# Kernel tuning notes

Measured on AMD Instinct MI355X. Metric: run time of the kernel, lower is better.

The kernel has to match this reference:

```python
import jax, jax.numpy as jnp
import numpy as np

B, C, L = 8, 2048, 256          # batch, seq (EEG channels), feature length
E = 3 * L                        # embed_dim = 768 (fused QKV width)
H = 4                            # attention heads
D = E // (3 * H)                 # head_dim = 64
SCALE = 8.0                      # hardcoded in the module (== sqrt(D) here)


def _layer_norm(x, gamma, beta, eps=1e-5):
    mu = jnp.mean(x, axis=-1, keepdims=True)
    var = jnp.var(x, axis=-1, keepdims=True)
    return (x - mu) * jax.lax.rsqrt(var + eps) * gamma + beta


def setup_inputs() -> dict:
    key = jax.random.key(0)
    ks = jax.random.split(key, 5)
    x = jax.random.normal(ks[0], (B, C, L), dtype=jnp.float32)
    # layers_1: Linear(L -> E) + LayerNorm(E)
    W1 = jax.random.normal(ks[1], (L, E), dtype=jnp.float32) / np.sqrt(L)
    b1 = jnp.zeros((E,), dtype=jnp.float32)
    g1 = jnp.ones((E,), dtype=jnp.float32)
    beta1 = jnp.zeros((E,), dtype=jnp.float32)
    # layers_2: Linear(L -> L) + LayerNorm(L)
    W2 = jax.random.normal(ks[2], (L, L), dtype=jnp.float32) / np.sqrt(L)
    b2 = jnp.zeros((L,), dtype=jnp.float32)
    g2 = jnp.ones((L,), dtype=jnp.float32)
    beta2 = jnp.zeros((L,), dtype=jnp.float32)
    return {"x": x, "W1": W1, "b1": b1, "g1": g1, "beta1": beta1,
            "W2": W2, "b2": b2, "g2": g2, "beta2": beta2}


def reference(x, W1, b1, g1, beta1, W2, b2, g2, beta2):
    b, c, _ = x.shape
    # layers_1 (dropout is identity in eval mode)
    y = _layer_norm(x @ W1 + b1, g1, beta1)                     # [b, c, E]
    qkv = y.reshape(b, c, 3, H, D).transpose(2, 0, 3, 1, 4)     # [3, b, H, c, D]
    q, k, v = qkv[0], qkv[1], qkv[2]
    attn = jax.nn.softmax(jnp.einsum('bhqd,bhkd->bhqk', q, k) / SCALE, axis=-1)
    o = jnp.einsum('bhqk,bhkd->bhqd', attn, v)                  # [b, H, c, D]
    o = o.transpose(0, 2, 1, 3).reshape(b, c, H * D)            # [b, c, L]
    # layers_2 + residual
    z = _layer_norm(o @ W2 + b2, g2, beta2) + x
    return z
```

## Files before the change

### kernel.cpp

```cpp
#include <hip/hip_runtime.h>
#include <hip/hip_bf16.h>

#define B_ 8
#define C_ 2048
#define L_ 256
#define E_ 768
#define H_ 4
#define D_ 64
#define M_ (B_*C_)

typedef __attribute__((ext_vector_type(8))) short short8v;
typedef __attribute__((ext_vector_type(4))) short short4v;
typedef __attribute__((ext_vector_type(4))) float f32x4;

__device__ __forceinline__ short f2bf(float f) {
  union { float f; unsigned u; } v; v.f = f;
  unsigned r = v.u + 0x7FFFu + ((v.u >> 16) & 1u);
  return (short)(r >> 16);
}
__device__ __forceinline__ unsigned cvtpk(float a, float b) {
  unsigned r;
  asm("v_cvt_pk_bf16_f32 %0, %1, %2" : "=v"(r) : "v"(a), "v"(b));
  return r;
}
__device__ __forceinline__ float exp2x(float x) {
  float r;
  asm("v_exp_f32 %0, %1" : "=v"(r) : "v"(x));
  return r;
}

__device__ __forceinline__ void gll16(const void* g, void* l) {
  __builtin_amdgcn_global_load_lds(
      (const __attribute__((address_space(1))) unsigned int*)g,
      (__attribute__((address_space(3))) unsigned int*)l, 16, 0, 0);
}

__global__ __launch_bounds__(256) void transpose_w_kernel(
    const float* __restrict__ W1, short* __restrict__ W1t,
    const float* __restrict__ W2, short* __restrict__ W2t) {
  __shared__ float ld[32][33];
  const int isW1 = blockIdx.y < 24;
  const float* W = isW1 ? W1 : W2;
  short* Wt = isW1 ? W1t : W2t;
  const int N = isW1 ? E_ : L_;
  const int k0 = blockIdx.x * 32, n0 = (isW1 ? blockIdx.y : blockIdx.y - 24) * 32;
  const int tx = threadIdx.x & 31, ty = threadIdx.x >> 5;
  #pragma unroll
  for (int j = 0; j < 4; ++j)
    ld[ty + j*8][tx] = W[(size_t)(k0 + ty + j*8) * N + n0 + tx];
  __syncthreads();
  const int r  = threadIdx.x >> 3;
  const int c0 = (threadIdx.x & 7) * 4;
  short4v o;
  o[0]=f2bf(ld[c0+0][r]); o[1]=f2bf(ld[c0+1][r]);
  o[2]=f2bf(ld[c0+2][r]); o[3]=f2bf(ld[c0+3][r]);
  *(short4v*)(Wt + (size_t)(n0 + r) * 256 + k0 + c0) = o;
}

__global__ __launch_bounds__(512, 2) void gemm1_ln_fused_kernel(
    const float* __restrict__ x, const short* __restrict__ W1t,
    const float* __restrict__ b1, const float* __restrict__ g1,
    const float* __restrict__ be1,
    short* __restrict__ Qg, short* __restrict__ Kg, short* __restrict__ Vtg) {
  __shared__ short As[32*264];
  __shared__ float2 red[8][32];
  __shared__ float mu_s[32], rs_s[32];
  const int tid = threadIdx.x;
  const int w = tid >> 6, l = tid & 63, lo = l & 15, hi = l >> 4;
  const int m0 = blockIdx.x * 32;
  const int b = m0 >> 11, c0 = m0 & (C_ - 1);
  const int nbase = w * 96;

  {
    const int row = tid >> 4, cc = (tid & 15) * 16;
    const float* ap = x + (size_t)(m0 + row) * 256 + cc;
    float4 a0 = ((const float4*)ap)[0], a1 = ((const float4*)ap)[1];
    float4 a2 = ((const float4*)ap)[2], a3 = ((const float4*)ap)[3];
    uint4 p0, p1;
    p0.x = cvtpk(a0.x,a0.y); p0.y = cvtpk(a0.z,a0.w);
    p0.z = cvtpk(a1.x,a1.y); p0.w = cvtpk(a1.z,a1.w);
    p1.x = cvtpk(a2.x,a2.y); p1.y = cvtpk(a2.z,a2.w);
    p1.z = cvtpk(a3.x,a3.y); p1.w = cvtpk(a3.z,a3.w);
    *(uint4*)&As[row*264 + cc]     = p0;
    *(uint4*)&As[row*264 + cc + 8] = p1;
  }
  __syncthreads();

  f32x4 acc[2][6];
  #pragma unroll
  for (int m = 0; m < 2; ++m)
    #pragma unroll
    for (int n = 0; n < 6; ++n) acc[m][n] = (f32x4){0.f,0.f,0.f,0.f};

  #pragma unroll
  for (int kt = 0; kt < 4; ++kt)
    #pragma unroll
    for (int kk = 0; kk < 2; ++kk) {
      short8v bf[6];
      #pragma unroll
      for (int n = 0; n < 6; ++n)
        bf[n] = *(const short8v*)(W1t + (size_t)(nbase + n*16 + lo) * 256
                                     + kt*64 + kk*32 + hi*8);
      short8v af0 = *(short8v*)&As[lo*264      + kt*64 + kk*32 + hi*8];
      short8v af1 = *(short8v*)&As[(16+lo)*264 + kt*64 + kk*32 + hi*8];
      #pragma unroll
      for (int n = 0; n < 6; ++n) {
        acc[0][n] = __builtin_amdgcn_mfma_f32_16x16x32_bf16(af0, bf[n], acc[0][n], 0,0,0);
        acc[1][n] = __builtin_amdgcn_mfma_f32_16x16x32_bf16(af1, bf[n], acc[1][n], 0,0,0);
      }
    }

  float bb[6], ggv[6], eev[6];
  #pragma unroll
  for (int n = 0; n < 6; ++n) {
    int col = nbase + n*16 + lo;
    bb[n] = b1[col]; ggv[n] = g1[col]; eev[n] = be1[col];
  }
  #pragma unroll
  for (int m = 0; m < 2; ++m)
    #pragma unroll
    for (int r = 0; r < 4; ++r) {
      float s = 0.f, s2 = 0.f;
      #pragma unroll
      for (int n = 0; n < 6; ++n) {
        float v = acc[m][n][r] + bb[n];
        acc[m][n][r] = v;
        s += v; s2 += v*v;
      }
      #pragma unroll
      for (int off = 1; off < 16; off <<= 1) {
        s  += __shfl_xor(s, off);
        s2 += __shfl_xor(s2, off);
      }
      if (lo == 0) red[w][m*16 + hi*4 + r] = make_float2(s, s2);
    }
  __syncthreads();
  if (tid < 32) {
    float s = 0.f, s2 = 0.f;
    #pragma unroll
    for (int wv = 0; wv < 8; ++wv) { s += red[wv][tid].x; s2 += red[wv][tid].y; }
    float mu = s * (1.f / E_);
    float var = s2 * (1.f / E_) - mu * mu;
    mu_s[tid] = mu;
    rs_s[tid] = rsqrtf(var + 1e-5f);
  }
  __syncthreads();

  const float qs = 0.18033688011f;
  #pragma unroll
  for (int m = 0; m < 2; ++m) {
    float mu4[4], rs4[4];
    #pragma unroll
    for (int r = 0; r < 4; ++r) {
      int row = m*16 + hi*4 + r;
      mu4[r] = mu_s[row]; rs4[r] = rs_s[row];
    }
    const int cbase = c0 + m*16 + hi*4;
    #pragma unroll
    for (int n = 0; n < 6; ++n) {
      const int e0 = nbase + n*16 + lo;
      float vals[4];
      #pragma unroll
      for (int r = 0; r < 4; ++r)
        vals[r] = (acc[m][n][r] - mu4[r]) * rs4[r] * ggv[n] + eev[n];
      if (e0 < 256) {
        const int h = e0 >> 6, d = e0 & 63;
        short* base = Qg + ((size_t)(b*H_ + h) * C_) * D_ + d;
        #pragma unroll
        for (int r = 0; r < 4; ++r)
          base[(size_t)(cbase + r) * D_] = f2bf(vals[r] * qs);
      } else if (e0 < 512) {
        const int eb = e0 - 256, h = eb >> 6, d = eb & 63;
        short* base = Kg + ((size_t)(b*H_ + h) * C_) * D_;
        #pragma unroll
        for (int r = 0; r < 4; ++r) {
          int c = cbase + r;
          base[(size_t)c * D_ + (((d>>3) ^ (c&7)) << 3) + (d&7)] = f2bf(vals[r]);
        }
      } else {
        const int eb = e0 - 512, h = eb >> 6, d = eb & 63;
        short4v pk;
        #pragma unroll
        for (int r = 0; r < 4; ++r) pk[r] = f2bf(vals[r]);
        const int c = cbase;
        size_t off = ((size_t)(b*H_ + h) * D_ + d) * C_ + (c & ~63)
                   + ((((c & 63) >> 3) ^ (d & 7)) << 3) + (c & 7);
        *(short4v*)(Vtg + off) = pk;
      }
    }
  }
}

__global__ __launch_bounds__(512, 4) void attn_mfma_kernel(
    const short* __restrict__ Qg, const short* __restrict__ Kg,
    const short* __restrict__ Vtg, short* __restrict__ ob) {
  __shared__ short Ks[3][4096];
  __shared__ short Vs[3][4096];
  __shared__ short Ps[8][1024];
  const int tid = threadIdx.x;
  const int w  = tid >> 6;
  const int l  = tid & 63, lo = l & 15, hi = l >> 4;
  const int sw = lo & 7;
  const int bh = blockIdx.x, qt = blockIdx.y;
  const size_t hd = (size_t)bh * (C_ * D_);
  const int q0 = qt * 128 + w * 16;

  const short8v bq0 = *(const short8v*)(Qg + hd + (size_t)(q0+lo)*D_ + hi*8);
  const short8v bq1 = *(const short8v*)(Qg + hd + (size_t)(q0+lo)*D_ + 32 + hi*8);

  short8v ones;
  #pragma unroll
  for (int j = 0; j < 8; ++j) ones[j] = (short)0x3F80;

  const short* Ktile = Kg + hd;
  const short* Vrow  = Vtg + hd;
  const int kOff = w*512 + l*8;
  const size_t vOff = (size_t)(w*8 + (l>>3)) * C_ + (l&7)*8;

  f32x4 Oacc[4] = {{0,0,0,0},{0,0,0,0},{0,0,0,0},{0,0,0,0}};
  f32x4 Lacc = {0.f, 0.f, 0.f, 0.f};
  const f32x4 zero4 = {0.f, 0.f, 0.f, 0.f};
  short* Pw = &Ps[w][0];

  gll16(Ktile + kOff, &Ks[0][w*512]);
  gll16(Vrow + vOff,  &Vs[0][w*512]);

  int cur = 0, nxt = 1;
  for (int kt = 0; kt < 32; ++kt) {
    asm volatile("s_waitcnt vmcnt(0)" ::: "memory");
    __builtin_amdgcn_s_barrier();
    if (kt != 31) {
      const short* kn = Ktile + (size_t)(kt+1) * 4096;
      const short* vn = Vrow  + (size_t)(kt+1) * 64;
      gll16(kn + kOff, &Ks[nxt][w*512]);
      gll16(vn + vOff, &Vs[nxt][w*512]);
    }
    const short* Kc = &Ks[cur][0];
    const short* Vc = &Vs[cur][0];

    f32x4 st[4];
    __builtin_amdgcn_s_setprio(1);
    #pragma unroll
    for (int mt = 0; mt < 4; ++mt) {
      short8v ka = *(const short8v*)&Kc[(mt*16 + lo)*64 + ((hi ^ sw) << 3)];
      short8v kb = *(const short8v*)&Kc[(mt*16 + lo)*64 + (((4 + hi) ^ sw) << 3)];
      f32x4 z = __builtin_amdgcn_mfma_f32_16x16x32_bf16(ka, bq0, zero4, 0, 0, 0);
      st[mt]  = __builtin_amdgcn_mfma_f32_16x16x32_bf16(kb, bq1, z, 0, 0, 0);
    }
    __builtin_amdgcn_s_setprio(0);

    float ps[16];
    #pragma unroll
    for (int mt = 0; mt < 4; ++mt)
      #pragma unroll
      for (int r = 0; r < 4; ++r)
        ps[mt*4 + r] = exp2x(st[mt][r]);

    #pragma unroll
    for (int mt = 0; mt < 4; ++mt) {
      uint2 pk;
      pk.x = cvtpk(ps[mt*4+0], ps[mt*4+1]);
      pk.y = cvtpk(ps[mt*4+2], ps[mt*4+3]);
      *(uint2*)&Pw[lo*64 + ((((mt<<1) + (hi>>1)) ^ sw) << 3) + ((hi&1) << 2)] = pk;
    }
    asm volatile("s_waitcnt lgkmcnt(0)" ::: "memory");

    short8v pa0 = *(short8v*)&Pw[lo*64 + ((hi ^ sw) << 3)];
    short8v pa1 = *(short8v*)&Pw[lo*64 + (((4 + hi) ^ sw) << 3)];
    __builtin_amdgcn_s_setprio(1);
    Lacc = __builtin_amdgcn_mfma_f32_16x16x32_bf16(pa0, ones, Lacc, 0, 0, 0);
    Lacc = __builtin_amdgcn_mfma_f32_16x16x32_bf16(pa1, ones, Lacc, 0, 0, 0);
    #pragma unroll
    for (int nt = 0; nt < 4; ++nt) {
      short8v vb0 = *(const short8v*)&Vc[(nt*16 + lo)*64 + ((hi ^ sw) << 3)];
      short8v vb1 = *(const short8v*)&Vc[(nt*16 + lo)*64 + (((4 + hi) ^ sw) << 3)];
      Oacc[nt] = __builtin_amdgcn_mfma_f32_16x16x32_bf16(pa0, vb0, Oacc[nt], 0,0,0);
      Oacc[nt] = __builtin_amdgcn_mfma_f32_16x16x32_bf16(pa1, vb1, Oacc[nt], 0,0,0);
    }
    __builtin_amdgcn_s_setprio(0);
    cur = nxt;
    nxt = (nxt == 2) ? 0 : nxt + 1;
  }

  float invL[4];
  #pragma unroll
  for (int r = 0; r < 4; ++r) invL[r] = 1.f / Lacc[r];
  const int b = bh >> 2, h = bh & 3;
  short* obp = ob + ((size_t)b * C_ + q0) * L_ + h * D_;
  #pragma unroll
  for (int nt = 0; nt < 4; ++nt)
    #pragma unroll
    for (int r = 0; r < 4; ++r)
      obp[(hi*4 + r) * L_ + nt*16 + lo] = f2bf(Oacc[nt][r] * invL[r]);
}

__global__ __launch_bounds__(256, 4) void gemm2_ln_mfma_kernel(
    const short* __restrict__ ob, const short* __restrict__ W2t,
    const float* __restrict__ b2, const float* __restrict__ g2,
    const float* __restrict__ be2, const float* __restrict__ x,
    float* __restrict__ out) {
  __shared__ short As[32*264];
  __shared__ float2 red[4][32];
  __shared__ float mu_s[32], rs_s[32];
  const int tid = threadIdx.x;
  const int w = tid >> 6, l = tid & 63, lo = l & 15, hi = l >> 4;
  const int m0 = blockIdx.x * 32;
  const int nbase = w * 64;

  #pragma unroll
  for (int i = 0; i < 4; ++i) {
    int id = tid + i * 256;
    int row = id >> 5, c8 = (id & 31) * 8;
    *(short8v*)&As[row*264 + c8] =
        *(const short8v*)(ob + (size_t)(m0 + row) * 256 + c8);
  }
  __syncthreads();

  f32x4 acc[2][4];
  #pragma unroll
  for (int m = 0; m < 2; ++m)
    #pragma unroll
    for (int n = 0; n < 4; ++n) acc[m][n] = (f32x4){0.f,0.f,0.f,0.f};

  #pragma unroll
  for (int kt = 0; kt < 4; ++kt)
    #pragma unroll
    for (int kk = 0; kk < 2; ++kk) {
      short8v bf[4];
      #pragma unroll
      for (int n = 0; n < 4; ++n)
        bf[n] = *(const short8v*)(W2t + (size_t)(nbase + n*16 + lo) * 256
                                     + kt*64 + kk*32 + hi*8);
      short8v af0 = *(short8v*)&As[lo*264      + kt*64 + kk*32 + hi*8];
      short8v af1 = *(short8v*)&As[(16+lo)*264 + kt*64 + kk*32 + hi*8];
      #pragma unroll
      for (int n = 0; n < 4; ++n) {
        acc[0][n] = __builtin_amdgcn_mfma_f32_16x16x32_bf16(af0, bf[n], acc[0][n], 0,0,0);
        acc[1][n] = __builtin_amdgcn_mfma_f32_16x16x32_bf16(af1, bf[n], acc[1][n], 0,0,0);
      }
    }

  float bb[4], gg[4], ee[4];
  #pragma unroll
  for (int n = 0; n < 4; ++n) {
    int col = nbase + n*16 + lo;
    bb[n] = b2[col]; gg[n] = g2[col]; ee[n] = be2[col];
  }
  #pragma unroll
  for (int m = 0; m < 2; ++m)
    #pragma unroll
    for (int r = 0; r < 4; ++r) {
      float s = 0.f, s2 = 0.f;
      #pragma unroll
      for (int n = 0; n < 4; ++n) {
        float v = acc[m][n][r] + bb[n];
        acc[m][n][r] = v;
        s += v; s2 += v*v;
      }
      #pragma unroll
      for (int off = 1; off < 16; off <<= 1) {
        s  += __shfl_xor(s, off);
        s2 += __shfl_xor(s2, off);
      }
      if (lo == 0) red[w][m*16 + hi*4 + r] = make_float2(s, s2);
    }
  __syncthreads();
  if (tid < 32) {
    float s = 0.f, s2 = 0.f;
    #pragma unroll
    for (int wv = 0; wv < 4; ++wv) { s += red[wv][tid].x; s2 += red[wv][tid].y; }
    float mu = s * (1.f / L_);
    float var = s2 * (1.f / L_) - mu * mu;
    mu_s[tid] = mu;
    rs_s[tid] = rsqrtf(var + 1e-5f);
  }
  __syncthreads();

  #pragma unroll
  for (int m = 0; m < 2; ++m) {
    float mu4[4], rs4[4];
    #pragma unroll
    for (int r = 0; r < 4; ++r) {
      int row = m*16 + hi*4 + r;
      mu4[r] = mu_s[row]; rs4[r] = rs_s[row];
    }
    #pragma unroll
    for (int r = 0; r < 4; ++r) {
      const int grow = m0 + m*16 + hi*4 + r;
      const float* xr = x + (size_t)grow * L_ + nbase;
      float* orow = out + (size_t)grow * L_ + nbase;
      #pragma unroll
      for (int n = 0; n < 4; ++n)
        orow[n*16 + lo] = (acc[m][n][r] - mu4[r]) * rs4[r] * gg[n] + ee[n]
                        + xr[n*16 + lo];
    }
  }
}

extern "C" void kernel_launch(void* const* d_in, const int* in_sizes, int n_in,
                              void* d_out, int out_size, void* d_ws, size_t ws_size,
                              hipStream_t stream) {
  const float* x   = (const float*)d_in[0];
  const float* W1  = (const float*)d_in[1];
  const float* b1  = (const float*)d_in[2];
  const float* g1  = (const float*)d_in[3];
  const float* be1 = (const float*)d_in[4];
  const float* W2  = (const float*)d_in[5];
  const float* b2  = (const float*)d_in[6];
  const float* g2  = (const float*)d_in[7];
  const float* be2 = (const float*)d_in[8];
  float* out = (float*)d_out;

  const size_t HDSZ = (size_t)B_ * H_ * C_ * D_;
  short* W1t = (short*)d_ws;
  short* W2t = W1t + (size_t)L_ * E_;
  short* Qg  = W2t + (size_t)L_ * L_;
  short* Kg  = Qg  + HDSZ;
  short* Vtg = Kg  + HDSZ;
  short* obm = Vtg + HDSZ;

  transpose_w_kernel<<<dim3(8, 32), 256, 0, stream>>>(W1, W1t, W2, W2t);
  gemm1_ln_fused_kernel<<<M_ / 32, 512, 0, stream>>>(x, W1t, b1, g1, be1, Qg, Kg, Vtg);
  attn_mfma_kernel<<<dim3(32, C_ / 128), 512, 0, stream>>>(Qg, Kg, Vtg, obm);
  gemm2_ln_mfma_kernel<<<M_ / 32, 256, 0, stream>>>(obm, W2t, b2, g2, be2, x, out);
}
```

Measured before the change: 103.6 us.

## Split attention key range across two blocks and merge partials in GEMM2

The attention kernel gains a third grid dimension that splits the 32 key tiles into two halves of 16. Each block writes its unnormalized partial output as bf16, plus its row sums, to separate workspace slots. GEMM2 then sums the two partials, divides by the combined row sum while loading its A tile, and continues as before. This doubles the number of attention blocks to fill more of the GPU, at the cost of extra workspace traffic and a second bf16 rounding of the partial outputs.

```diff
diff --git a/kernel.cpp b/kernel.cpp
--- a/kernel.cpp
+++ b/kernel.cpp
@@ -17,6 +17,10 @@
   union { float f; unsigned u; } v; v.f = f;
   unsigned r = v.u + 0x7FFFu + ((v.u >> 16) & 1u);
   return (short)(r >> 16);
+}
+__device__ __forceinline__ float bf2f(short s) {
+  union { unsigned u; float f; } v; v.u = ((unsigned)(unsigned short)s) << 16;
+  return v.f;
 }
 __device__ __forceinline__ unsigned cvtpk(float a, float b) {
   unsigned r;
@@ -193,7 +197,8 @@
 
 __global__ __launch_bounds__(512, 4) void attn_mfma_kernel(
     const short* __restrict__ Qg, const short* __restrict__ Kg,
-    const short* __restrict__ Vtg, short* __restrict__ ob) {
+    const short* __restrict__ Vtg, short* __restrict__ obm,
+    float* __restrict__ lg) {
   __shared__ short Ks[3][4096];
   __shared__ short Vs[3][4096];
   __shared__ short Ps[8][1024];
@@ -201,9 +206,10 @@
   const int w  = tid >> 6;
   const int l  = tid & 63, lo = l & 15, hi = l >> 4;
   const int sw = lo & 7;
-  const int bh = blockIdx.x, qt = blockIdx.y;
+  const int bh = blockIdx.x, qt = blockIdx.y, ks = blockIdx.z;
   const size_t hd = (size_t)bh * (C_ * D_);
   const int q0 = qt * 128 + w * 16;
+  const int kt0 = ks * 16;
 
   const short8v bq0 = *(const short8v*)(Qg + hd + (size_t)(q0+lo)*D_ + hi*8);
   const short8v bq1 = *(const short8v*)(Qg + hd + (size_t)(q0+lo)*D_ + 32 + hi*8);
@@ -212,8 +218,8 @@
   #pragma unroll
   for (int j = 0; j < 8; ++j) ones[j] = (short)0x3F80;
 
-  const short* Ktile = Kg + hd;
-  const short* Vrow  = Vtg + hd;
+  const short* Ktile = Kg + hd + (size_t)kt0 * 4096;
+  const short* Vrow  = Vtg + hd + (size_t)kt0 * 64;
   const int kOff = w*512 + l*8;
   const size_t vOff = (size_t)(w*8 + (l>>3)) * C_ + (l&7)*8;
 
@@ -226,12 +232,12 @@
   gll16(Vrow + vOff,  &Vs[0][w*512]);
 
   int cur = 0, nxt = 1;
-  for (int kt = 0; kt < 32; ++kt) {
+  for (int ktl = 0; ktl < 16; ++ktl) {
     asm volatile("s_waitcnt vmcnt(0)" ::: "memory");
     __builtin_amdgcn_s_barrier();
-    if (kt != 31) {
-      const short* kn = Ktile + (size_t)(kt+1) * 4096;
-      const short* vn = Vrow  + (size_t)(kt+1) * 64;
+    if (ktl != 15) {
+      const short* kn = Ktile + (size_t)(ktl+1) * 4096;
+      const short* vn = Vrow  + (size_t)(ktl+1) * 64;
       gll16(kn + kOff, &Ks[nxt][w*512]);
       gll16(vn + vOff, &Vs[nxt][w*512]);
     }
@@ -282,20 +288,23 @@
     nxt = (nxt == 2) ? 0 : nxt + 1;
   }
 
-  float invL[4];
-  #pragma unroll
-  for (int r = 0; r < 4; ++r) invL[r] = 1.f / Lacc[r];
   const int b = bh >> 2, h = bh & 3;
-  short* obp = ob + ((size_t)b * C_ + q0) * L_ + h * D_;
+  short* obp = obm + (size_t)ks * (M_ * L_) + ((size_t)b * C_ + q0) * L_ + h * D_;
   #pragma unroll
   for (int nt = 0; nt < 4; ++nt)
     #pragma unroll
     for (int r = 0; r < 4; ++r)
-      obp[(hi*4 + r) * L_ + nt*16 + lo] = f2bf(Oacc[nt][r] * invL[r]);
+      obp[(hi*4 + r) * L_ + nt*16 + lo] = f2bf(Oacc[nt][r]);
+  if (lo == 0) {
+    float* lp = lg + ((size_t)ks * 32 + bh) * C_ + q0;
+    #pragma unroll
+    for (int r = 0; r < 4; ++r) lp[hi*4 + r] = Lacc[r];
+  }
 }
 
 __global__ __launch_bounds__(256, 4) void gemm2_ln_mfma_kernel(
-    const short* __restrict__ ob, const short* __restrict__ W2t,
+    const short* __restrict__ obm, const float* __restrict__ lg,
+    const short* __restrict__ W2t,
     const float* __restrict__ b2, const float* __restrict__ g2,
     const float* __restrict__ be2, const float* __restrict__ x,
     float* __restrict__ out) {
@@ -305,14 +314,25 @@
   const int tid = threadIdx.x;
   const int w = tid >> 6, l = tid & 63, lo = l & 15, hi = l >> 4;
   const int m0 = blockIdx.x * 32;
+  const int bb_ = m0 >> 11, cb = m0 & (C_ - 1);
   const int nbase = w * 64;
 
   #pragma unroll
   for (int i = 0; i < 4; ++i) {
     int id = tid + i * 256;
     int row = id >> 5, c8 = (id & 31) * 8;
-    *(short8v*)&As[row*264 + c8] =
-        *(const short8v*)(ob + (size_t)(m0 + row) * 256 + c8);
+    int h = c8 >> 6;
+    size_t goff = (size_t)(m0 + row) * 256 + c8;
+    short8v o1 = *(const short8v*)(obm + goff);
+    short8v o2 = *(const short8v*)(obm + (size_t)(M_ * L_) + goff);
+    float l1 = lg[(size_t)(bb_*4 + h) * C_ + cb + row];
+    float l2 = lg[(size_t)(32 + bb_*4 + h) * C_ + cb + row];
+    float inv = 1.f / (l1 + l2);
+    short8v o;
+    #pragma unroll
+    for (int j = 0; j < 8; ++j)
+      o[j] = f2bf((bf2f(o1[j]) + bf2f(o2[j])) * inv);
+    *(short8v*)&As[row*264 + c8] = o;
   }
   __syncthreads();
 
@@ -418,9 +438,10 @@
   short* Kg  = Qg  + HDSZ;
   short* Vtg = Kg  + HDSZ;
   short* obm = Vtg + HDSZ;
+  float* lg  = (float*)(obm + 2 * (size_t)M_ * L_);
 
   transpose_w_kernel<<<dim3(8, 32), 256, 0, stream>>>(W1, W1t, W2, W2t);
   gemm1_ln_fused_kernel<<<M_ / 32, 512, 0, stream>>>(x, W1t, b1, g1, be1, Qg, Kg, Vtg);
-  attn_mfma_kernel<<<dim3(32, C_ / 128), 512, 0, stream>>>(Qg, Kg, Vtg, obm);
-  gemm2_ln_mfma_kernel<<<M_ / 32, 256, 0, stream>>>(obm, W2t, b2, g2, be2, x, out);
-}
+  attn_mfma_kernel<<<dim3(32, C_ / 128, 2), 512, 0, stream>>>(Qg, Kg, Vtg, obm, lg);
+  gemm2_ln_mfma_kernel<<<M_ / 32, 256, 0, stream>>>(obm, lg, W2t, b2, g2, be2, x, out);
+}
```

Measured after the change: 106.2 us. 1.03x slower.

## Software-pipeline QK^T one tile ahead with four-deep K/V LDS ring

Applied to the files above, without the earlier changes.

Restructures the attention loop so the QK^T MFMAs for tile kt+1 are issued before the exp/pack and PV work of tile kt. The K/V LDS ring grows from three to four buffers, and prefetch now runs two tiles ahead. The aim is to overlap the exp/convert VALU work and LDS round-trips with matrix-core work, and to hide more global load latency. In exchange it needs 16KB more shared memory and extra live registers for the second score buffer. That could lower occupancy or cause spills.

```diff
diff --git a/kernel.cpp b/kernel.cpp
--- a/kernel.cpp
+++ b/kernel.cpp
@@ -194,8 +194,8 @@
 __global__ __launch_bounds__(512, 4) void attn_mfma_kernel(
     const short* __restrict__ Qg, const short* __restrict__ Kg,
     const short* __restrict__ Vtg, short* __restrict__ ob) {
-  __shared__ short Ks[3][4096];
-  __shared__ short Vs[3][4096];
+  __shared__ short Ks[4][4096];
+  __shared__ short Vs[4][4096];
   __shared__ short Ps[8][1024];
   const int tid = threadIdx.x;
   const int w  = tid >> 6;
@@ -222,24 +222,15 @@
   const f32x4 zero4 = {0.f, 0.f, 0.f, 0.f};
   short* Pw = &Ps[w][0];
 
-  gll16(Ktile + kOff, &Ks[0][w*512]);
-  gll16(Vrow + vOff,  &Vs[0][w*512]);
-
-  int cur = 0, nxt = 1;
-  for (int kt = 0; kt < 32; ++kt) {
-    asm volatile("s_waitcnt vmcnt(0)" ::: "memory");
-    __builtin_amdgcn_s_barrier();
-    if (kt != 31) {
-      const short* kn = Ktile + (size_t)(kt+1) * 4096;
-      const short* vn = Vrow  + (size_t)(kt+1) * 64;
-      gll16(kn + kOff, &Ks[nxt][w*512]);
-      gll16(vn + vOff, &Vs[nxt][w*512]);
-    }
-    const short* Kc = &Ks[cur][0];
-    const short* Vc = &Vs[cur][0];
-
-    f32x4 st[4];
-    __builtin_amdgcn_s_setprio(1);
+  gll16(Ktile + kOff,        &Ks[0][w*512]);
+  gll16(Vrow + vOff,         &Vs[0][w*512]);
+  gll16(Ktile + 4096 + kOff, &Ks[1][w*512]);
+  gll16(Vrow + 64 + vOff,    &Vs[1][w*512]);
+  asm volatile("s_waitcnt vmcnt(2)" ::: "memory");
+  __builtin_amdgcn_s_barrier();
+  f32x4 st[4], stN[4];
+  {
+    const short* Kc = &Ks[0][0];
     #pragma unroll
     for (int mt = 0; mt < 4; ++mt) {
       short8v ka = *(const short8v*)&Kc[(mt*16 + lo)*64 + ((hi ^ sw) << 3)];
@@ -247,7 +238,29 @@
       f32x4 z = __builtin_amdgcn_mfma_f32_16x16x32_bf16(ka, bq0, zero4, 0, 0, 0);
       st[mt]  = __builtin_amdgcn_mfma_f32_16x16x32_bf16(kb, bq1, z, 0, 0, 0);
     }
-    __builtin_amdgcn_s_setprio(0);
+  }
+
+  for (int kt = 0; kt < 32; ++kt) {
+    asm volatile("s_waitcnt vmcnt(0)" ::: "memory");
+    __builtin_amdgcn_s_barrier();
+    if (kt < 30) {
+      const short* kn = Ktile + (size_t)(kt+2) * 4096;
+      const short* vn = Vrow  + (size_t)(kt+2) * 64;
+      gll16(kn + kOff, &Ks[(kt+2)&3][w*512]);
+      gll16(vn + vOff, &Vs[(kt+2)&3][w*512]);
+    }
+    if (kt < 31) {
+      const short* Kc = &Ks[(kt+1)&3][0];
+      __builtin_amdgcn_s_setprio(1);
+      #pragma unroll
+      for (int mt = 0; mt < 4; ++mt) {
+        short8v ka = *(const short8v*)&Kc[(mt*16 + lo)*64 + ((hi ^ sw) << 3)];
+        short8v kb = *(const short8v*)&Kc[(mt*16 + lo)*64 + (((4 + hi) ^ sw) << 3)];
+        f32x4 z = __builtin_amdgcn_mfma_f32_16x16x32_bf16(ka, bq0, zero4, 0, 0, 0);
+        stN[mt] = __builtin_amdgcn_mfma_f32_16x16x32_bf16(kb, bq1, z, 0, 0, 0);
+      }
+      __builtin_amdgcn_s_setprio(0);
+    }
 
     float ps[16];
     #pragma unroll
@@ -267,6 +280,7 @@
 
     short8v pa0 = *(short8v*)&Pw[lo*64 + ((hi ^ sw) << 3)];
     short8v pa1 = *(short8v*)&Pw[lo*64 + (((4 + hi) ^ sw) << 3)];
+    const short* Vc = &Vs[kt&3][0];
     __builtin_amdgcn_s_setprio(1);
     Lacc = __builtin_amdgcn_mfma_f32_16x16x32_bf16(pa0, ones, Lacc, 0, 0, 0);
     Lacc = __builtin_amdgcn_mfma_f32_16x16x32_bf16(pa1, ones, Lacc, 0, 0, 0);
@@ -278,8 +292,8 @@
       Oacc[nt] = __builtin_amdgcn_mfma_f32_16x16x32_bf16(pa1, vb1, Oacc[nt], 0,0,0);
     }
     __builtin_amdgcn_s_setprio(0);
-    cur = nxt;
-    nxt = (nxt == 2) ? 0 : nxt + 1;
+    #pragma unroll
+    for (int m = 0; m < 4; ++m) st[m] = stN[m];
   }
 
   float invL[4];
```

Measured after the change: 104.5 us. No clear change (+0.8%).
